# Kernel optimization log

Measured on AMD Instinct MI355X. Metric: run time of the kernel, lower is better.

## Reference

```python
import jax, jax.numpy as jnp
import numpy as np

N = 4096        # batch_size per view
D = 256         # embed_dim
TEMPERATURE = 0.1


def setup_inputs() -> dict:
    key = jax.random.key(0)
    k1, k2 = jax.random.split(key)
    return {
        "z_i": jax.random.normal(k1, (N, D), dtype=jnp.float32),
        "z_j": jax.random.normal(k2, (N, D), dtype=jnp.float32),
    }


def reference(z_i, z_j):
    n = z_i.shape[0]
    # L2-normalize each row (CosineSimilarity == dot of normalized vectors)
    zi = z_i * jax.lax.rsqrt(jnp.sum(z_i * z_i, axis=1, keepdims=True))
    zj = z_j * jax.lax.rsqrt(jnp.sum(z_j * z_j, axis=1, keepdims=True))
    r = jnp.concatenate([zj, zi], axis=0)               # [2n, d], order matches torch cat([z_j, z_i])
    S = (r @ r.T) / TEMPERATURE                          # [2n, 2n] normalized GEMM, no O(n^2 d) broadcast

    idx = jnp.arange(2 * n)
    pos_col = (idx + n) % (2 * n)                        # positive partner: diag(+n) / diag(-n)
    pos = S[idx, pos_col]                                # [2n]

    # Faithful mask: the original masks the diagonal AND both full cross blocks,
    # so negatives are same-view off-diagonal entries only. Keep = negatives + positive.
    same_block = (idx[:, None] // n) == (idx[None, :] // n)
    keep = (same_block & (idx[:, None] != idx[None, :])) | (idx[None, :] == pos_col[:, None])

    # CrossEntropy with label 0 and reduction='sum', then / (2n)  ==  mean(logsumexp - pos)
    lse = jax.nn.logsumexp(jnp.where(keep, S, -jnp.inf), axis=1)  # [2n]
    return jnp.mean(lse - pos)
```

## Files before the change

kernel.cpp:

```cpp
#include <hip/hip_runtime.h>
#include <math.h>

#define N_ROWS 4096
#define DIM 256
constexpr float INV_T = 10.0f;

#define NT 32
#define NTILES 528
#define BM 128
#define BK 64
#define PSTRIDE 512

typedef __attribute__((ext_vector_type(8))) short short8;
typedef __attribute__((ext_vector_type(4))) float floatx4;

typedef __attribute__((address_space(3))) unsigned int lds_uint;
typedef const __attribute__((address_space(1))) unsigned int glb_uint;

__device__ __forceinline__ unsigned short f2bf(float f) {
    unsigned int u = __float_as_uint(f);
    return (unsigned short)((u + 0x7FFFu + ((u >> 16) & 1u)) >> 16);
}

__global__ __launch_bounds__(256) void normalize_kernel(
    const float* __restrict__ z_i, const float* __restrict__ z_j,
    unsigned short* __restrict__ R0, unsigned short* __restrict__ R1,
    float* __restrict__ pos, float* __restrict__ out)
{
    if (blockIdx.x == 0 && threadIdx.x == 0) out[0] = 0.0f;

    int wave = threadIdx.x >> 6;
    int lane = threadIdx.x & 63;
    int row = blockIdx.x * 4 + wave;

    float4 a = ((const float4*)(z_i + (size_t)row * DIM))[lane];
    float4 b = ((const float4*)(z_j + (size_t)row * DIM))[lane];

    float ssa = a.x*a.x + a.y*a.y + a.z*a.z + a.w*a.w;
    float ssb = b.x*b.x + b.y*b.y + b.z*b.z + b.w*b.w;
    float dab = a.x*b.x + a.y*b.y + a.z*b.z + a.w*b.w;
    #pragma unroll
    for (int off = 1; off < 64; off <<= 1) {
        ssa += __shfl_xor(ssa, off);
        ssb += __shfl_xor(ssb, off);
        dab += __shfl_xor(dab, off);
    }
    float ra = rsqrtf(ssa);
    float rb = rsqrtf(ssb);

    ushort4 ua, ub;
    ua.x = f2bf(a.x * ra); ua.y = f2bf(a.y * ra); ua.z = f2bf(a.z * ra); ua.w = f2bf(a.w * ra);
    ub.x = f2bf(b.x * rb); ub.y = f2bf(b.y * rb); ub.z = f2bf(b.z * rb); ub.w = f2bf(b.w * rb);
    ((ushort4*)(R1 + (size_t)row * DIM))[lane] = ua;
    ((ushort4*)(R0 + (size_t)row * DIM))[lane] = ub;

    if (lane == 0) pos[row] = dab * ra * rb * INV_T;
}

__global__ __launch_bounds__(256, 4) void gemm_sym(
    const unsigned short* __restrict__ R0,
    const unsigned short* __restrict__ R1,
    float* __restrict__ part)
{
    __shared__ unsigned short As[BM * BK];
    __shared__ unsigned short Bs[BM * BK];

    int view = blockIdx.y;
    const unsigned short* R = view ? R1 : R0;
    float* P = part + (size_t)(view * NTILES + blockIdx.x) * PSTRIDE;

    int t = blockIdx.x;
    int by = 0;
    while (t >= NT - by) { t -= NT - by; ++by; }
    int bx = by + t;
    int rT = by * BM, cT = bx * BM;

    int tid = threadIdx.x;
    int lane = tid & 63;
    int wave = tid >> 6;
    int wy = wave >> 1, wx = wave & 1;
    int m = lane & 15, q = lane >> 4;

    floatx4 acc[4][4] = {};

    for (int kidx = 0; kidx < 4; ++kidx) {
        int k0 = kidx * BK;
        __syncthreads();
        #pragma unroll
        for (int stp = 0; stp < 4; ++stp) {
            int s = stp * 256 + tid;
            int row = s >> 3, p = s & 7;
            int cg = p ^ (row & 7);
            const unsigned short* ga = R + (size_t)(rT + row) * DIM + k0 + cg * 8;
            const unsigned short* gb = R + (size_t)(cT + row) * DIM + k0 + cg * 8;
            __builtin_amdgcn_global_load_lds((glb_uint*)ga, (lds_uint*)&As[s * 8], 16, 0, 0);
            __builtin_amdgcn_global_load_lds((glb_uint*)gb, (lds_uint*)&Bs[s * 8], 16, 0, 0);
        }
        __syncthreads();

        #pragma unroll
        for (int kk = 0; kk < 2; ++kk) {
            short8 af[4], bfr[4];
            #pragma unroll
            for (int tt = 0; tt < 4; ++tt) {
                int ra = wy * 64 + tt * 16 + m;
                af[tt] = *(const short8*)&As[(ra * 8 + ((kk * 4 + q) ^ (ra & 7))) * 8];
                int rb = wx * 64 + tt * 16 + m;
                bfr[tt] = *(const short8*)&Bs[(rb * 8 + ((kk * 4 + q) ^ (rb & 7))) * 8];
            }
            #pragma unroll
            for (int i = 0; i < 4; ++i)
                #pragma unroll
                for (int j = 0; j < 4; ++j)
                    acc[i][j] = __builtin_amdgcn_mfma_f32_16x16x32_bf16(af[i], bfr[j], acc[i][j], 0, 0, 0);
        }
    }

    float rs[4][4] = {};
    float cs[4] = {0.f, 0.f, 0.f, 0.f};
    #pragma unroll
    for (int i = 0; i < 4; ++i) {
        #pragma unroll
        for (int j = 0; j < 4; ++j) {
            int gcol = cT + wx * 64 + j * 16 + m;
            #pragma unroll
            for (int r = 0; r < 4; ++r) {
                int grow = rT + wy * 64 + i * 16 + q * 4 + r;
                float e = (grow == gcol) ? 0.0f : __expf(acc[i][j][r] * INV_T);
                rs[i][r] += e;
                cs[j] += e;
            }
        }
    }
    #pragma unroll
    for (int off = 1; off < 16; off <<= 1)
        #pragma unroll
        for (int i = 0; i < 4; ++i)
            #pragma unroll
            for (int r = 0; r < 4; ++r)
                rs[i][r] += __shfl_xor(rs[i][r], off);
    if (m == 0) {
        #pragma unroll
        for (int i = 0; i < 4; ++i) {
            float4 v = make_float4(rs[i][0], rs[i][1], rs[i][2], rs[i][3]);
            *(float4*)&P[wx * 128 + wy * 64 + i * 16 + q * 4] = v;
        }
    }
    #pragma unroll
    for (int off = 16; off < 64; off <<= 1)
        #pragma unroll
        for (int j = 0; j < 4; ++j)
            cs[j] += __shfl_xor(cs[j], off);
    if (q == 0) {
        #pragma unroll
        for (int j = 0; j < 4; ++j)
            P[256 + wy * 128 + wx * 64 + j * 16 + m] = (bx == by) ? 0.0f : cs[j];
    }
}

__global__ __launch_bounds__(256) void finalize_kernel(
    const float* __restrict__ part, const float* __restrict__ pos,
    float* __restrict__ out)
{
    int g = blockIdx.x * 256 + threadIdx.x;
    int v = g >> 12, r = g & (N_ROWS - 1);
    int b = r >> 7, l = r & 127;
    const float* P = part + (size_t)v * NTILES * PSTRIDE;

    float d = 0.f;
    int t0 = b * NT - (b * (b - 1)) / 2;
    for (int k = 0; k < NT - b; ++k) {
        const float* T = P + (size_t)(t0 + k) * PSTRIDE;
        d += T[l] + T[128 + l];
    }
    for (int by = 0; by <= b; ++by) {
        int tb = by * NT - (by * (by - 1)) / 2 + (b - by);
        const float* T = P + (size_t)tb * PSTRIDE;
        d += T[256 + l] + T[384 + l];
    }
    float p = pos[r];
    float s = __logf(d + __expf(p)) - p;
    #pragma unroll
    for (int off = 1; off < 64; off <<= 1) s += __shfl_xor(s, off);
    if ((threadIdx.x & 63) == 0)
        atomicAdd(out, s * (1.0f / (2 * N_ROWS)));
}

extern "C" void kernel_launch(void* const* d_in, const int* in_sizes, int n_in,
                              void* d_out, int out_size, void* d_ws, size_t ws_size,
                              hipStream_t stream) {
    const float* z_i = (const float*)d_in[0];
    const float* z_j = (const float*)d_in[1];
    char* ws = (char*)d_ws;
    unsigned short* R0 = (unsigned short*)ws;
    unsigned short* R1 = (unsigned short*)(ws + (2u << 20));
    float* pos  = (float*)(ws + (4u << 20));
    float* part = (float*)(ws + (4u << 20) + (64u << 10));

    normalize_kernel<<<N_ROWS / 4, 256, 0, stream>>>(z_i, z_j, R0, R1, pos,
                                                     (float*)d_out);
    dim3 grid(NTILES, 2);
    gemm_sym<<<grid, 256, 0, stream>>>(R0, R1, part);
    finalize_kernel<<<2 * N_ROWS / 256, 256, 0, stream>>>(part, pos, (float*)d_out);
}
```

Before: 89.83 us.

## Double-buffer LDS tiles in symmetric GEMM to overlap loads with MFMA

```diff
diff --git a/kernel.cpp b/kernel.cpp
--- a/kernel.cpp
+++ b/kernel.cpp
@@ -57,13 +57,13 @@
     if (lane == 0) pos[row] = dab * ra * rb * INV_T;
 }
 
-__global__ __launch_bounds__(256, 4) void gemm_sym(
+__global__ __launch_bounds__(256) void gemm_sym(
     const unsigned short* __restrict__ R0,
     const unsigned short* __restrict__ R1,
     float* __restrict__ part)
 {
-    __shared__ unsigned short As[BM * BK];
-    __shared__ unsigned short Bs[BM * BK];
+    __shared__ unsigned short As[2][BM * BK];
+    __shared__ unsigned short Bs[2][BM * BK];
 
     int view = blockIdx.y;
     const unsigned short* R = view ? R1 : R0;
@@ -81,11 +81,13 @@
     int wy = wave >> 1, wx = wave & 1;
     int m = lane & 15, q = lane >> 4;
 
+    int srow = tid >> 1;
+    (void)srow;
+
     floatx4 acc[4][4] = {};
 
-    for (int kidx = 0; kidx < 4; ++kidx) {
+    auto stage = [&](int kidx, int buf) {
         int k0 = kidx * BK;
-        __syncthreads();
         #pragma unroll
         for (int stp = 0; stp < 4; ++stp) {
             int s = stp * 256 + tid;
@@ -93,20 +95,30 @@
             int cg = p ^ (row & 7);
             const unsigned short* ga = R + (size_t)(rT + row) * DIM + k0 + cg * 8;
             const unsigned short* gb = R + (size_t)(cT + row) * DIM + k0 + cg * 8;
-            __builtin_amdgcn_global_load_lds((glb_uint*)ga, (lds_uint*)&As[s * 8], 16, 0, 0);
-            __builtin_amdgcn_global_load_lds((glb_uint*)gb, (lds_uint*)&Bs[s * 8], 16, 0, 0);
-        }
-        __syncthreads();
-
+            __builtin_amdgcn_global_load_lds((glb_uint*)ga, (lds_uint*)&As[buf][s * 8], 16, 0, 0);
+            __builtin_amdgcn_global_load_lds((glb_uint*)gb, (lds_uint*)&Bs[buf][s * 8], 16, 0, 0);
+        }
+    };
+
+    stage(0, 0);
+
+    #pragma unroll
+    for (int k = 0; k < 4; ++k) {
+        if (k < 3) stage(k + 1, (k + 1) & 1);
+        if (k < 3) asm volatile("s_waitcnt vmcnt(8)" ::: "memory");
+        else       asm volatile("s_waitcnt vmcnt(0)" ::: "memory");
+        asm volatile("s_barrier" ::: "memory");
+        const unsigned short* Ab = As[k & 1];
+        const unsigned short* Bb = Bs[k & 1];
         #pragma unroll
         for (int kk = 0; kk < 2; ++kk) {
             short8 af[4], bfr[4];
             #pragma unroll
             for (int tt = 0; tt < 4; ++tt) {
                 int ra = wy * 64 + tt * 16 + m;
-                af[tt] = *(const short8*)&As[(ra * 8 + ((kk * 4 + q) ^ (ra & 7))) * 8];
+                af[tt] = *(const short8*)&Ab[(ra * 8 + ((kk * 4 + q) ^ (ra & 7))) * 8];
                 int rb = wx * 64 + tt * 16 + m;
-                bfr[tt] = *(const short8*)&Bs[(rb * 8 + ((kk * 4 + q) ^ (rb & 7))) * 8];
+                bfr[tt] = *(const short8*)&Bb[(rb * 8 + ((kk * 4 + q) ^ (rb & 7))) * 8];
             }
             #pragma unroll
             for (int i = 0; i < 4; ++i)
@@ -114,6 +126,7 @@
                 for (int j = 0; j < 4; ++j)
                     acc[i][j] = __builtin_amdgcn_mfma_f32_16x16x32_bf16(af[i], bfr[j], acc[i][j], 0, 0, 0);
         }
+        if (k < 3) asm volatile("s_waitcnt lgkmcnt(0)\n\ts_barrier" ::: "memory");
     }
 
     float rs[4][4] = {};
```

Result: no change. 90.87 us (+1.2%).
